# Performance work log

Hardware: AMD Instinct MI355X
Metric: run time of the kernel (lower is better)

## Reference

```python
import jax, jax.numpy as jnp
import numpy as np

N_NODES = 10000
N_EDGES = 160000
NUM_FEAT = 14
EDGE_DIM = 4
DIM = 64        # hidden_channels
HID = 128       # GENConv MLP expansion = 2
LAYERS = 28
MSG_EPS = 1e-7  # GENConv eps added to relu(message)
LN_EPS = 1e-5   # torch LayerNorm default


def layernorm(h, g, b):
    mu = jnp.mean(h, axis=-1, keepdims=True)
    var = jnp.mean(jnp.square(h - mu), axis=-1, keepdims=True)
    return (h - mu) * jax.lax.rsqrt(var + LN_EPS) * g + b


def gen_conv(x, ea, src, dst, t, W1, b1, g1, be1, W2, b2):
    # message: relu(x_j + edge_attr) + eps  -> [E, D]
    msg = jax.nn.relu(x[src] + ea) + MSG_EPS
    # softmax aggregation over edges grouped by destination node
    logits = msg * t
    m = jax.ops.segment_max(logits, dst, num_segments=N_NODES)
    e = jnp.exp(logits - m[dst])
    s = jax.ops.segment_sum(e, dst, num_segments=N_NODES)
    alpha = e / (s[dst] + 1e-16)
    agg = jax.ops.segment_sum(msg * alpha, dst, num_segments=N_NODES)
    # residual + MLP [D -> 2D -> D] with LayerNorm+ReLU in between
    h = agg + x
    h = jax.nn.relu(layernorm(h @ W1 + b1, g1, be1))
    return h @ W2 + b2


def setup_inputs() -> dict:
    key = jax.random.key(0)
    ks = jax.random.split(key, 24)
    sc = 0.05
    inp = {
        "x": jax.random.normal(ks[0], (N_NODES, NUM_FEAT), jnp.float32),
        "edge_attr": jax.random.normal(ks[1], (N_EDGES, EDGE_DIM), jnp.float32),
        "src": jax.random.randint(ks[2], (N_EDGES,), 0, N_NODES, jnp.int32),
        "dst": jax.random.randint(ks[3], (N_EDGES,), 0, N_NODES, jnp.int32),
        # encoders
        "W_node": jax.random.normal(ks[4], (NUM_FEAT, DIM), jnp.float32) * sc,
        "b_node": jnp.zeros((DIM,), jnp.float32),
        "W_edge": jax.random.normal(ks[5], (EDGE_DIM, DIM), jnp.float32) * sc,
        "b_edge": jnp.zeros((DIM,), jnp.float32),
        # per-layer GENConv params (stacked over LAYERS)
        "t": jnp.ones((LAYERS,), jnp.float32),
        "W1": jax.random.normal(ks[6], (LAYERS, DIM, HID), jnp.float32) * sc,
        "b1": jnp.zeros((LAYERS, HID), jnp.float32),
        "g1": jnp.ones((LAYERS, HID), jnp.float32),
        "be1": jnp.zeros((LAYERS, HID), jnp.float32),
        "W2": jax.random.normal(ks[7], (LAYERS, HID, DIM), jnp.float32) * sc,
        "b2": jnp.zeros((LAYERS, DIM), jnp.float32),
        # per-layer DeepGCNLayer LayerNorm
        "ln_g": jnp.ones((LAYERS, DIM), jnp.float32),
        "ln_b": jnp.zeros((LAYERS, DIM), jnp.float32),
        # output projection
        "W_out": jax.random.normal(ks[8], (DIM, DIM), jnp.float32) * sc,
        "b_out": jnp.zeros((DIM,), jnp.float32),
    }
    return inp


def reference(x, edge_attr, src, dst, W_node, b_node, W_edge, b_edge,
              t, W1, b1, g1, be1, W2, b2, ln_g, ln_b, W_out, b_out):
    h = x @ W_node + b_node                  # node encoder  [N, D]
    ea = edge_attr @ W_edge + b_edge         # edge encoder  [E, D]

    # layer 0: conv only (no res+ wrapper), per DeeperGCN.forward
    h = gen_conv(h, ea, src, dst, t[0], W1[0], b1[0], g1[0], be1[0], W2[0], b2[0])

    # layers 1..L-1: res+ block: x + conv(dropout(relu(norm(x))))  (eval: dropout = id)
    def step(hc, p):
        ti, w1, bb1, gg1, bbe1, w2, bb2, lg, lb = p
        u = jax.nn.relu(layernorm(hc, lg, lb))
        u = gen_conv(u, ea, src, dst, ti, w1, bb1, gg1, bbe1, w2, bb2)
        return hc + u, None

    rest = (t[1:], W1[1:], b1[1:], g1[1:], be1[1:], W2[1:], b2[1:], ln_g[1:], ln_b[1:])
    h, _ = jax.lax.scan(step, h, rest)

    # final: act(layers[0].norm(x)), dropout (eval: id), lin
    h = jax.nn.relu(layernorm(h, ln_g[0], ln_b[0]))
    return h @ W_out + b_out
```

## Files before the change

kernel.cpp:

```cpp
#include <hip/hip_runtime.h>

#define N_NODES 10000
#define N_EDGES 160000
#define NUM_FEAT 14
#define EDGE_DIM 4
#define DIM 64
#define HID 128
#define LAYERS 28

#define NPB 20
#define NLB (N_NODES / NPB)
#define TPB 640

__device__ __forceinline__ void stage16(const float* gsrc, float* lds_base) {
  __builtin_amdgcn_global_load_lds(
      (const __attribute__((address_space(1))) void*)gsrc,
      (__attribute__((address_space(3))) void*)lds_base, 16, 0, 0);
}


__global__ __launch_bounds__(256) void k_hist(const int* __restrict__ dst, int* __restrict__ cur) {
  int e = blockIdx.x * 256 + threadIdx.x;
  if (e < N_EDGES) atomicAdd(&cur[dst[e]], 1);
}

__global__ __launch_bounds__(256) void k_scan(int* __restrict__ cur, int* __restrict__ off) {
  __shared__ int part[256];
  int t = threadIdx.x;
  const int CH = 40;
  int base = t * CH;
  int s = 0;
  for (int i = 0; i < CH; i++) {
    int idx = base + i;
    if (idx < N_NODES) s += cur[idx];
  }
  part[t] = s;
  __syncthreads();
  for (int ofs = 1; ofs < 256; ofs <<= 1) {
    int tmp = (t >= ofs) ? part[t - ofs] : 0;
    __syncthreads();
    part[t] += tmp;
    __syncthreads();
  }
  int run = part[t] - s;
  for (int i = 0; i < CH; i++) {
    int idx = base + i;
    if (idx < N_NODES) {
      int d = cur[idx];
      off[idx] = run;
      cur[idx] = run;
      run += d;
    }
  }
  if (t == 255) off[N_NODES] = part[255];
}

__global__ __launch_bounds__(256) void k_scatter(const int* __restrict__ dst, int* __restrict__ cur,
                                                 int* __restrict__ eids) {
  int e = blockIdx.x * 256 + threadIdx.x;
  if (e < N_EDGES) {
    int p = atomicAdd(&cur[dst[e]], 1);
    eids[p] = e;
  }
}

__global__ __launch_bounds__(256) void k_sortgather(
    const int* __restrict__ off, const int* __restrict__ eids,
    const int* __restrict__ src, const float4* __restrict__ eattr,
    int* __restrict__ src_s, float4* __restrict__ eattr_s) {
  int node = blockIdx.x * 4 + (threadIdx.x >> 6);
  int lane = threadIdx.x & 63;
  if (node >= N_NODES) return;
  int a = off[node];
  int d = off[node + 1] - a;
  if (d <= 64) {
    int key = (lane < d) ? eids[a + lane] : 0x7fffffff;
#pragma unroll
    for (int k = 2; k <= 64; k <<= 1) {
      for (int j = k >> 1; j > 0; j >>= 1) {
        int p = __shfl_xor(key, j);
        bool dirUp = ((lane & k) == 0);
        bool isLower = ((lane & j) == 0);
        key = ((isLower == dirUp) ? min(key, p) : max(key, p));
      }
    }
    if (lane < d) {
      src_s[a + lane] = src[key];
      eattr_s[a + lane] = eattr[key];
    }
  } else {
    for (int i = lane; i < d; i += 64) {
      int e = eids[a + i];
      int r = 0;
      for (int j = 0; j < d; j++) r += (eids[a + j] < e) ? 1 : 0;
      src_s[a + r] = src[e];
      eattr_s[a + r] = eattr[e];
    }
  }
}


__global__ __launch_bounds__(256) void k_enc(const float* __restrict__ x, const float* __restrict__ Wn,
                                             const float* __restrict__ bn, float* __restrict__ hc,
                                             float* __restrict__ u) {
  int gid = blockIdx.x * 256 + threadIdx.x;
  if (gid >= N_NODES * DIM) return;
  int n = gid >> 6, j = gid & 63;
  float acc = bn[j];
#pragma unroll
  for (int k = 0; k < NUM_FEAT; k++) acc += x[n * NUM_FEAT + k] * Wn[k * DIM + j];
  hc[gid] = acc;
  u[gid] = acc;
}

__device__ __forceinline__ float edge_node(
    int gn, const float* __restrict__ uin, const float4* __restrict__ eattr_s,
    const int* __restrict__ src_s, const int* __restrict__ off,
    int lane, float tv, float we0, float we1, float we2, float we3, float be) {
  int a = off[gn], d = off[gn + 1] - a;
  float un = uin[(gn << 6) + lane];
  float s0 = 0.f, s1 = 0.f, ac0 = 0.f, ac1 = 0.f;
  int nb = d & ~7;
  float uv[8], ep[8];
  if (nb > 0) {
#pragma unroll
    for (int j = 0; j < 8; j++) {
      int sn = src_s[a + j];
      uv[j] = uin[(sn << 6) + lane];
      float4 ev = eattr_s[a + j];
      ep[j] = be + ev.x * we0 + ev.y * we1 + ev.z * we2 + ev.w * we3;
    }
  }
  for (int i = 0; i < nb; i += 8) {
    float uvn[8], epn[8];
    const bool more = (i + 8) < nb;
    if (more) {
#pragma unroll
      for (int j = 0; j < 8; j++) {
        int sn = src_s[a + i + 8 + j];
        uvn[j] = uin[(sn << 6) + lane];
        float4 ev = eattr_s[a + i + 8 + j];
        epn[j] = be + ev.x * we0 + ev.y * we1 + ev.z * we2 + ev.w * we3;
      }
    }
#pragma unroll
    for (int j = 0; j < 8; j++) {
      float msg = fmaxf(uv[j] + ep[j], 0.f) + 1e-7f;
      float e = __expf(msg * tv);
      if (j & 1) { s1 += e; ac1 = fmaf(e, msg, ac1); }
      else       { s0 += e; ac0 = fmaf(e, msg, ac0); }
    }
    if (more) {
#pragma unroll
      for (int j = 0; j < 8; j++) { uv[j] = uvn[j]; ep[j] = epn[j]; }
    }
  }
  for (int i = nb; i < d; i++) {
    int sn = src_s[a + i];
    float4 ev = eattr_s[a + i];
    float epp = be + ev.x * we0 + ev.y * we1 + ev.z * we2 + ev.w * we3;
    float msg = fmaxf(uin[(sn << 6) + lane] + epp, 0.f) + 1e-7f;
    float e = __expf(msg * tv);
    s0 += e;
    ac0 = fmaf(e, msg, ac0);
  }
  return (ac0 + ac1) / (s0 + s1 + 1e-16f) + un;
}


__global__ __launch_bounds__(640, 5) void k_layer(
    const float* __restrict__ uin, float* __restrict__ hc, float* __restrict__ uout,
    const float4* __restrict__ eattr_s, const int* __restrict__ src_s,
    const int* __restrict__ off, const float* __restrict__ tptr, int layer,
    const float* __restrict__ W_edge, const float* __restrict__ b_edge,
    const float* __restrict__ W1, const float* __restrict__ b1,
    const float* __restrict__ g1, const float* __restrict__ be1,
    const float* __restrict__ W2, const float* __restrict__ b2,
    const float* __restrict__ lng, const float* __restrict__ lnb,
    int addRes, int writeU) {
  __shared__ float sW1[64 * 128];
  __shared__ float sW2[128 * 64];
  __shared__ float sHZ[10][256];

  const int tid = threadIdx.x;
  const int lane = tid & 63;
  const int wv = tid >> 6;
  const int nbase = blockIdx.x * NPB;

  for (int c = wv; c < 32; c += 10) {
    stage16(W1 + c * 256 + lane * 4, sW1 + c * 256);
    stage16(W2 + c * 256 + lane * 4, sW2 + c * 256);
  }

  {
    float tv = tptr[layer];
    float we0 = W_edge[lane], we1 = W_edge[64 + lane], we2 = W_edge[128 + lane],
          we3 = W_edge[192 + lane];
    float be = b_edge[lane];
    int gn0 = __builtin_amdgcn_readfirstlane(nbase + wv * 2);
    float h0 = edge_node(gn0, uin, eattr_s, src_s, off, lane, tv, we0, we1, we2, we3, be);
    float h1 = edge_node(gn0 + 1, uin, eattr_s, src_s, off, lane, tv, we0, we1, we2, we3, be);
    *((float2*)&sHZ[wv][lane * 2]) = make_float2(h0, h1);
  }
  __syncthreads();

  const int gn0 = nbase + wv * 2;
  const int gn1 = gn0 + 1;

  int j0 = 2 * lane;
  float2 b1v = *((const float2*)&b1[j0]);
  float a00 = b1v.x, a01 = b1v.y, a10 = b1v.x, a11 = b1v.y;
#pragma unroll 8
  for (int k = 0; k < 64; k++) {
    float2 hp = *((float2*)&sHZ[wv][k * 2]);
    float2 wp = *((float2*)&sW1[k * 128 + j0]);
    a00 += hp.x * wp.x; a01 += hp.x * wp.y;
    a10 += hp.y * wp.x; a11 += hp.y * wp.y;
  }

  {
    float2 gv = *((const float2*)&g1[j0]);
    float2 bev = *((const float2*)&be1[j0]);
    float s0 = a00 + a01, q0 = a00 * a00 + a01 * a01;
    float s1 = a10 + a11, q1 = a10 * a10 + a11 * a11;
#pragma unroll
    for (int o = 32; o; o >>= 1) {
      s0 += __shfl_xor(s0, o); q0 += __shfl_xor(q0, o);
      s1 += __shfl_xor(s1, o); q1 += __shfl_xor(q1, o);
    }
    float mu0 = s0 * (1.f / 128.f), mu1 = s1 * (1.f / 128.f);
    float rs0 = rsqrtf(q0 * (1.f / 128.f) - mu0 * mu0 + 1e-5f);
    float rs1 = rsqrtf(q1 * (1.f / 128.f) - mu1 * mu1 + 1e-5f);
    float4 zv;
    zv.x = fmaxf((a00 - mu0) * rs0 * gv.x + bev.x, 0.f);
    zv.y = fmaxf((a10 - mu1) * rs1 * gv.x + bev.x, 0.f);
    zv.z = fmaxf((a01 - mu0) * rs0 * gv.y + bev.y, 0.f);
    zv.w = fmaxf((a11 - mu1) * rs1 * gv.y + bev.y, 0.f);
    *((float4*)&sHZ[wv][4 * lane]) = zv;
  }

  float bo = b2[lane];
  float o0 = bo, o1 = bo;
#pragma unroll 8
  for (int k = 0; k < 128; k++) {
    float2 zp = *((float2*)&sHZ[wv][k * 2]);
    float wv2 = sW2[k * 64 + lane];
    o0 += zp.x * wv2;
    o1 += zp.y * wv2;
  }

  float r0 = addRes ? hc[gn0 * 64 + lane] : 0.f;
  float r1 = addRes ? hc[gn1 * 64 + lane] : 0.f;
  float hcn0 = o0 + r0, hcn1 = o1 + r1;
  hc[gn0 * 64 + lane] = hcn0;
  hc[gn1 * 64 + lane] = hcn1;

  if (writeU) {
    float lg_ = lng[lane], lb_ = lnb[lane];
    float s0 = hcn0, q0 = hcn0 * hcn0;
    float s1 = hcn1, q1 = hcn1 * hcn1;
#pragma unroll
    for (int o = 32; o; o >>= 1) {
      s0 += __shfl_xor(s0, o); q0 += __shfl_xor(q0, o);
      s1 += __shfl_xor(s1, o); q1 += __shfl_xor(q1, o);
    }
    float mu0 = s0 * (1.f / 64.f), mu1 = s1 * (1.f / 64.f);
    float rs0 = rsqrtf(q0 * (1.f / 64.f) - mu0 * mu0 + 1e-5f);
    float rs1 = rsqrtf(q1 * (1.f / 64.f) - mu1 * mu1 + 1e-5f);
    uout[gn0 * 64 + lane] = fmaxf((hcn0 - mu0) * rs0 * lg_ + lb_, 0.f);
    uout[gn1 * 64 + lane] = fmaxf((hcn1 - mu1) * rs1 * lg_ + lb_, 0.f);
  }
}


__global__ __launch_bounds__(256) void k_final(const float* __restrict__ hc, const float* __restrict__ g,
                                               const float* __restrict__ bptr, const float* __restrict__ Wout,
                                               const float* __restrict__ bout, float* __restrict__ out) {
  __shared__ float sW[DIM * DIM];
  int tid = threadIdx.x;
  for (int i = tid; i < 1024; i += 256) ((float4*)sW)[i] = ((const float4*)Wout)[i];
  __syncthreads();
  int lane = tid & 63, w = tid >> 6;
  int n = blockIdx.x * 4 + w;
  if (n >= N_NODES) return;
  float v = hc[n * 64 + lane];
  float s = v, q = v * v;
#pragma unroll
  for (int o = 32; o; o >>= 1) { s += __shfl_xor(s, o); q += __shfl_xor(q, o); }
  float mu = s * (1.f / 64.f);
  float var = q * (1.f / 64.f) - mu * mu;
  float rs = rsqrtf(var + 1e-5f);
  float z = fmaxf((v - mu) * rs * g[lane] + bptr[lane], 0.f);
  float acc = bout[lane];
  for (int k = 0; k < 64; k++) {
    float zk = __shfl(z, k);
    acc += zk * sW[k * 64 + lane];
  }
  out[n * 64 + lane] = acc;
}


extern "C" void kernel_launch(void* const* d_in, const int* in_sizes, int n_in,
                              void* d_out, int out_size, void* d_ws, size_t ws_size,
                              hipStream_t stream) {
  const float* x        = (const float*)d_in[0];
  const float* eattr    = (const float*)d_in[1];
  const int*   src      = (const int*)d_in[2];
  const int*   dst      = (const int*)d_in[3];
  const float* W_node   = (const float*)d_in[4];
  const float* b_node   = (const float*)d_in[5];
  const float* W_edge   = (const float*)d_in[6];
  const float* b_edge   = (const float*)d_in[7];
  const float* t        = (const float*)d_in[8];
  const float* W1       = (const float*)d_in[9];
  const float* b1       = (const float*)d_in[10];
  const float* g1       = (const float*)d_in[11];
  const float* be1      = (const float*)d_in[12];
  const float* W2       = (const float*)d_in[13];
  const float* b2       = (const float*)d_in[14];
  const float* ln_g     = (const float*)d_in[15];
  const float* ln_b     = (const float*)d_in[16];
  const float* W_out    = (const float*)d_in[17];
  const float* b_out    = (const float*)d_in[18];
  float* out = (float*)d_out;

  char* w = (char*)d_ws;
  float* uA      = (float*)w;  w += (size_t)N_NODES * 64 * 4;
  float* uB      = (float*)w;  w += (size_t)N_NODES * 64 * 4;
  float* hcb     = (float*)w;  w += (size_t)N_NODES * 64 * 4;
  int* off       = (int*)w;    w += (size_t)(N_NODES + 1) * 4;
  int* cur       = (int*)w;    w += (size_t)N_NODES * 4;
  int* eids      = (int*)w;    w += (size_t)N_EDGES * 4;
  int* src_s     = (int*)w;    w += (size_t)N_EDGES * 4;
  float4* eattr_s = (float4*)w; w += (size_t)N_EDGES * 16;

  hipMemsetAsync(cur, 0, (size_t)N_NODES * 4, stream);
  k_hist<<<(N_EDGES + 255) / 256, 256, 0, stream>>>(dst, cur);
  k_scan<<<1, 256, 0, stream>>>(cur, off);
  k_scatter<<<(N_EDGES + 255) / 256, 256, 0, stream>>>(dst, cur, eids);
  k_sortgather<<<(N_NODES + 3) / 4, 256, 0, stream>>>(off, eids, src, (const float4*)eattr,
                                                      src_s, eattr_s);

  k_enc<<<(N_NODES * 64 + 255) / 256, 256, 0, stream>>>(x, W_node, b_node, hcb, uA);

  for (int l = 0; l < LAYERS; l++) {
    const float* uin = (l & 1) ? uB : uA;
    float* uo        = (l & 1) ? uA : uB;
    int nxt = (l + 1 < LAYERS) ? (l + 1) : 0;
    k_layer<<<NLB, TPB, 0, stream>>>(uin, hcb, uo, (const float4*)eattr_s, src_s, off, t, l,
                                     W_edge, b_edge,
                                     W1 + (size_t)l * DIM * HID, b1 + (size_t)l * HID,
                                     g1 + (size_t)l * HID, be1 + (size_t)l * HID,
                                     W2 + (size_t)l * HID * DIM, b2 + (size_t)l * DIM,
                                     ln_g + (size_t)nxt * DIM, ln_b + (size_t)nxt * DIM,
                                     (l > 0) ? 1 : 0, (l < LAYERS - 1) ? 1 : 0);
  }

  k_final<<<(N_NODES + 3) / 4, 256, 0, stream>>>(hcb, ln_g, ln_b, W_out, b_out, out);
}
```

Measured before the change: 848.8 us.

## Pair nodes per wave by degree rank to balance edge-aggregation work

Adds a counting sort of nodes by in-degree (histogram, scan, rank) run once before the layer loop. Each wave in the layer kernel now processes one low-degree node and its mirror high-degree node from the sorted list instead of two consecutive nodes. This is meant to even out per-wave edge-loop lengths so waves in a block reach the barrier together. In exchange it adds three small setup kernels, an indirection load per wave, and scattered node addresses, which weaken the locality of the node-state reads and writes.

```diff
diff --git a/kernel.cpp b/kernel.cpp
--- a/kernel.cpp
+++ b/kernel.cpp
@@ -11,6 +11,7 @@
 #define NPB 20
 #define NLB (N_NODES / NPB)
 #define TPB 640
+#define NBUCK 128
 
 __device__ __forceinline__ void stage16(const float* gsrc, float* lds_base) {
   __builtin_amdgcn_global_load_lds(
@@ -100,6 +101,41 @@
 }
 
 
+__global__ __launch_bounds__(256) void k_dbucket(const int* __restrict__ off, int* __restrict__ dh) {
+  int n = blockIdx.x * 256 + threadIdx.x;
+  if (n < N_NODES) {
+    int d = off[n + 1] - off[n];
+    if (d > NBUCK - 1) d = NBUCK - 1;
+    atomicAdd(&dh[d], 1);
+  }
+}
+
+__global__ __launch_bounds__(NBUCK) void k_dscan(const int* __restrict__ dh, int* __restrict__ dcur) {
+  __shared__ int v[NBUCK];
+  int t = threadIdx.x;
+  v[t] = dh[t];
+  __syncthreads();
+  for (int o = 1; o < NBUCK; o <<= 1) {
+    int tmp = (t >= o) ? v[t - o] : 0;
+    __syncthreads();
+    v[t] += tmp;
+    __syncthreads();
+  }
+  dcur[t] = v[t] - dh[t];
+}
+
+__global__ __launch_bounds__(256) void k_drank(const int* __restrict__ off, int* __restrict__ dcur,
+                                               int* __restrict__ snode) {
+  int n = blockIdx.x * 256 + threadIdx.x;
+  if (n < N_NODES) {
+    int d = off[n + 1] - off[n];
+    if (d > NBUCK - 1) d = NBUCK - 1;
+    int r = atomicAdd(&dcur[d], 1);
+    snode[r] = n;
+  }
+}
+
+
 __global__ __launch_bounds__(256) void k_enc(const float* __restrict__ x, const float* __restrict__ Wn,
                                              const float* __restrict__ bn, float* __restrict__ hc,
                                              float* __restrict__ u) {
@@ -171,7 +207,8 @@
 __global__ __launch_bounds__(640, 5) void k_layer(
     const float* __restrict__ uin, float* __restrict__ hc, float* __restrict__ uout,
     const float4* __restrict__ eattr_s, const int* __restrict__ src_s,
-    const int* __restrict__ off, const float* __restrict__ tptr, int layer,
+    const int* __restrict__ off, const int* __restrict__ snode,
+    const float* __restrict__ tptr, int layer,
     const float* __restrict__ W_edge, const float* __restrict__ b_edge,
     const float* __restrict__ W1, const float* __restrict__ b1,
     const float* __restrict__ g1, const float* __restrict__ be1,
@@ -185,7 +222,9 @@
   const int tid = threadIdx.x;
   const int lane = tid & 63;
   const int wv = tid >> 6;
-  const int nbase = blockIdx.x * NPB;
+  const int slot = blockIdx.x * 10 + wv;
+  const int gn0 = __builtin_amdgcn_readfirstlane(snode[slot]);
+  const int gn1 = __builtin_amdgcn_readfirstlane(snode[N_NODES - 1 - slot]);
 
   for (int c = wv; c < 32; c += 10) {
     stage16(W1 + c * 256 + lane * 4, sW1 + c * 256);
@@ -197,15 +236,11 @@
     float we0 = W_edge[lane], we1 = W_edge[64 + lane], we2 = W_edge[128 + lane],
           we3 = W_edge[192 + lane];
     float be = b_edge[lane];
-    int gn0 = __builtin_amdgcn_readfirstlane(nbase + wv * 2);
     float h0 = edge_node(gn0, uin, eattr_s, src_s, off, lane, tv, we0, we1, we2, we3, be);
-    float h1 = edge_node(gn0 + 1, uin, eattr_s, src_s, off, lane, tv, we0, we1, we2, we3, be);
+    float h1 = edge_node(gn1, uin, eattr_s, src_s, off, lane, tv, we0, we1, we2, we3, be);
     *((float2*)&sHZ[wv][lane * 2]) = make_float2(h0, h1);
   }
   __syncthreads();
-
-  const int gn0 = nbase + wv * 2;
-  const int gn1 = gn0 + 1;
 
   int j0 = 2 * lane;
   float2 b1v = *((const float2*)&b1[j0]);
@@ -333,13 +368,20 @@
   int* eids      = (int*)w;    w += (size_t)N_EDGES * 4;
   int* src_s     = (int*)w;    w += (size_t)N_EDGES * 4;
   float4* eattr_s = (float4*)w; w += (size_t)N_EDGES * 16;
+  int* dh        = (int*)w;    w += (size_t)NBUCK * 4;
+  int* dcur      = (int*)w;    w += (size_t)NBUCK * 4;
+  int* snode     = (int*)w;    w += (size_t)N_NODES * 4;
 
   hipMemsetAsync(cur, 0, (size_t)N_NODES * 4, stream);
+  hipMemsetAsync(dh, 0, (size_t)NBUCK * 4, stream);
   k_hist<<<(N_EDGES + 255) / 256, 256, 0, stream>>>(dst, cur);
   k_scan<<<1, 256, 0, stream>>>(cur, off);
   k_scatter<<<(N_EDGES + 255) / 256, 256, 0, stream>>>(dst, cur, eids);
   k_sortgather<<<(N_NODES + 3) / 4, 256, 0, stream>>>(off, eids, src, (const float4*)eattr,
                                                       src_s, eattr_s);
+  k_dbucket<<<(N_NODES + 255) / 256, 256, 0, stream>>>(off, dh);
+  k_dscan<<<1, NBUCK, 0, stream>>>(dh, dcur);
+  k_drank<<<(N_NODES + 255) / 256, 256, 0, stream>>>(off, dcur, snode);
 
   k_enc<<<(N_NODES * 64 + 255) / 256, 256, 0, stream>>>(x, W_node, b_node, hcb, uA);
 
@@ -347,8 +389,8 @@
     const float* uin = (l & 1) ? uB : uA;
     float* uo        = (l & 1) ? uA : uB;
     int nxt = (l + 1 < LAYERS) ? (l + 1) : 0;
-    k_layer<<<NLB, TPB, 0, stream>>>(uin, hcb, uo, (const float4*)eattr_s, src_s, off, t, l,
-                                     W_edge, b_edge,
+    k_layer<<<NLB, TPB, 0, stream>>>(uin, hcb, uo, (const float4*)eattr_s, src_s, off, snode,
+                                     t, l, W_edge, b_edge,
                                      W1 + (size_t)l * DIM * HID, b1 + (size_t)l * HID,
                                      g1 + (size_t)l * HID, be1 + (size_t)l * HID,
                                      W2 + (size_t)l * HID * DIM, b2 + (size_t)l * DIM,
```

New measurement: 912.8 us. 7.5% more time.

## Use one node per wave and read W2 from global to cut LDS use

Applied to the files above, without the earlier changes.

Each wave now processes one node instead of two, with 8 waves of 512 threads per block covering 8 nodes, and occupancy raised to 8 blocks per CU. W2 is no longer staged in LDS. It is read straight from global memory or cache in the second MLP matmul, which cuts shared memory roughly in half so more blocks fit. The trade-off is more weight reloads per node, since W1 staging is amortised over fewer nodes, and W2 reads now come from cache instead of LDS. In exchange there is more parallelism to hide the latency of the irregular edge gather.

```diff
diff --git a/kernel.cpp b/kernel.cpp
--- a/kernel.cpp
+++ b/kernel.cpp
@@ -8,9 +8,9 @@
 #define HID 128
 #define LAYERS 28
 
-#define NPB 20
+#define NPB 8
 #define NLB (N_NODES / NPB)
-#define TPB 640
+#define TPB 512
 
 __device__ __forceinline__ void stage16(const float* gsrc, float* lds_base) {
   __builtin_amdgcn_global_load_lds(
@@ -168,7 +168,7 @@
 }
 
 
-__global__ __launch_bounds__(640, 5) void k_layer(
+__global__ __launch_bounds__(512, 8) void k_layer(
     const float* __restrict__ uin, float* __restrict__ hc, float* __restrict__ uout,
     const float4* __restrict__ eattr_s, const int* __restrict__ src_s,
     const int* __restrict__ off, const float* __restrict__ tptr, int layer,
@@ -179,17 +179,15 @@
     const float* __restrict__ lng, const float* __restrict__ lnb,
     int addRes, int writeU) {
   __shared__ float sW1[64 * 128];
-  __shared__ float sW2[128 * 64];
-  __shared__ float sHZ[10][256];
+  __shared__ float sHZ[8][128];
 
   const int tid = threadIdx.x;
   const int lane = tid & 63;
   const int wv = tid >> 6;
-  const int nbase = blockIdx.x * NPB;
-
-  for (int c = wv; c < 32; c += 10) {
+  const int gn = __builtin_amdgcn_readfirstlane(blockIdx.x * NPB + wv);
+
+  for (int c = wv; c < 32; c += 8) {
     stage16(W1 + c * 256 + lane * 4, sW1 + c * 256);
-    stage16(W2 + c * 256 + lane * 4, sW2 + c * 256);
   }
 
   {
@@ -197,78 +195,55 @@
     float we0 = W_edge[lane], we1 = W_edge[64 + lane], we2 = W_edge[128 + lane],
           we3 = W_edge[192 + lane];
     float be = b_edge[lane];
-    int gn0 = __builtin_amdgcn_readfirstlane(nbase + wv * 2);
-    float h0 = edge_node(gn0, uin, eattr_s, src_s, off, lane, tv, we0, we1, we2, we3, be);
-    float h1 = edge_node(gn0 + 1, uin, eattr_s, src_s, off, lane, tv, we0, we1, we2, we3, be);
-    *((float2*)&sHZ[wv][lane * 2]) = make_float2(h0, h1);
+    float h = edge_node(gn, uin, eattr_s, src_s, off, lane, tv, we0, we1, we2, we3, be);
+    sHZ[wv][lane] = h;
   }
   __syncthreads();
-
-  const int gn0 = nbase + wv * 2;
-  const int gn1 = gn0 + 1;
 
   int j0 = 2 * lane;
   float2 b1v = *((const float2*)&b1[j0]);
-  float a00 = b1v.x, a01 = b1v.y, a10 = b1v.x, a11 = b1v.y;
+  float a0 = b1v.x, a1 = b1v.y;
 #pragma unroll 8
   for (int k = 0; k < 64; k++) {
-    float2 hp = *((float2*)&sHZ[wv][k * 2]);
+    float h = sHZ[wv][k];
     float2 wp = *((float2*)&sW1[k * 128 + j0]);
-    a00 += hp.x * wp.x; a01 += hp.x * wp.y;
-    a10 += hp.y * wp.x; a11 += hp.y * wp.y;
+    a0 = fmaf(h, wp.x, a0);
+    a1 = fmaf(h, wp.y, a1);
   }
 
   {
     float2 gv = *((const float2*)&g1[j0]);
     float2 bev = *((const float2*)&be1[j0]);
-    float s0 = a00 + a01, q0 = a00 * a00 + a01 * a01;
-    float s1 = a10 + a11, q1 = a10 * a10 + a11 * a11;
-#pragma unroll
-    for (int o = 32; o; o >>= 1) {
-      s0 += __shfl_xor(s0, o); q0 += __shfl_xor(q0, o);
-      s1 += __shfl_xor(s1, o); q1 += __shfl_xor(q1, o);
-    }
-    float mu0 = s0 * (1.f / 128.f), mu1 = s1 * (1.f / 128.f);
-    float rs0 = rsqrtf(q0 * (1.f / 128.f) - mu0 * mu0 + 1e-5f);
-    float rs1 = rsqrtf(q1 * (1.f / 128.f) - mu1 * mu1 + 1e-5f);
-    float4 zv;
-    zv.x = fmaxf((a00 - mu0) * rs0 * gv.x + bev.x, 0.f);
-    zv.y = fmaxf((a10 - mu1) * rs1 * gv.x + bev.x, 0.f);
-    zv.z = fmaxf((a01 - mu0) * rs0 * gv.y + bev.y, 0.f);
-    zv.w = fmaxf((a11 - mu1) * rs1 * gv.y + bev.y, 0.f);
-    *((float4*)&sHZ[wv][4 * lane]) = zv;
-  }
-
-  float bo = b2[lane];
-  float o0 = bo, o1 = bo;
+    float s = a0 + a1, q = a0 * a0 + a1 * a1;
+#pragma unroll
+    for (int o = 32; o; o >>= 1) { s += __shfl_xor(s, o); q += __shfl_xor(q, o); }
+    float mu = s * (1.f / 128.f);
+    float rs = rsqrtf(q * (1.f / 128.f) - mu * mu + 1e-5f);
+    float2 zv;
+    zv.x = fmaxf((a0 - mu) * rs * gv.x + bev.x, 0.f);
+    zv.y = fmaxf((a1 - mu) * rs * gv.y + bev.y, 0.f);
+    *((float2*)&sHZ[wv][j0]) = zv;
+  }
+
+  float o = b2[lane];
 #pragma unroll 8
   for (int k = 0; k < 128; k++) {
-    float2 zp = *((float2*)&sHZ[wv][k * 2]);
-    float wv2 = sW2[k * 64 + lane];
-    o0 += zp.x * wv2;
-    o1 += zp.y * wv2;
-  }
-
-  float r0 = addRes ? hc[gn0 * 64 + lane] : 0.f;
-  float r1 = addRes ? hc[gn1 * 64 + lane] : 0.f;
-  float hcn0 = o0 + r0, hcn1 = o1 + r1;
-  hc[gn0 * 64 + lane] = hcn0;
-  hc[gn1 * 64 + lane] = hcn1;
+    float z = sHZ[wv][k];
+    o = fmaf(z, W2[k * 64 + lane], o);
+  }
+
+  float r = addRes ? hc[gn * 64 + lane] : 0.f;
+  float hcn = o + r;
+  hc[gn * 64 + lane] = hcn;
 
   if (writeU) {
     float lg_ = lng[lane], lb_ = lnb[lane];
-    float s0 = hcn0, q0 = hcn0 * hcn0;
-    float s1 = hcn1, q1 = hcn1 * hcn1;
-#pragma unroll
-    for (int o = 32; o; o >>= 1) {
-      s0 += __shfl_xor(s0, o); q0 += __shfl_xor(q0, o);
-      s1 += __shfl_xor(s1, o); q1 += __shfl_xor(q1, o);
-    }
-    float mu0 = s0 * (1.f / 64.f), mu1 = s1 * (1.f / 64.f);
-    float rs0 = rsqrtf(q0 * (1.f / 64.f) - mu0 * mu0 + 1e-5f);
-    float rs1 = rsqrtf(q1 * (1.f / 64.f) - mu1 * mu1 + 1e-5f);
-    uout[gn0 * 64 + lane] = fmaxf((hcn0 - mu0) * rs0 * lg_ + lb_, 0.f);
-    uout[gn1 * 64 + lane] = fmaxf((hcn1 - mu1) * rs1 * lg_ + lb_, 0.f);
+    float s = hcn, q = hcn * hcn;
+#pragma unroll
+    for (int o2 = 32; o2; o2 >>= 1) { s += __shfl_xor(s, o2); q += __shfl_xor(q, o2); }
+    float mu = s * (1.f / 64.f);
+    float rs = rsqrtf(q * (1.f / 64.f) - mu * mu + 1e-5f);
+    uout[gn * 64 + lane] = fmaxf((hcn - mu) * rs * lg_ + lb_, 0.f);
   }
 }
 
```

Result: no change. 836.7 us (-1.4%).
